# Performance work log

Measured on AMD Instinct MI355X. Metric: run time of the kernel, lower is better.

## Reference

```python
import jax, jax.numpy as jnp
import numpy as np

N, E, D, L, G, T = 50000, 600000, 128, 4, 512, 10
EPS = 1e-5


def setup_inputs() -> dict:
    key = jax.random.key(0)
    ks = jax.random.split(key, 20)
    s = lambda k, shp, fan: jax.random.normal(k, shp, jnp.float32) * (1.0 / np.sqrt(fan))
    inp = {
        'x': jax.random.normal(ks[0], (N, 3), jnp.float32),
        'edge_index': jax.random.randint(ks[1], (2, E), 0, N, jnp.int32),
        'batch': jnp.sort(jax.random.randint(ks[2], (N,), 0, G, jnp.int32)),
        'emb_W': s(ks[3], (3, D), 3),
        'emb_b': jnp.zeros((D,), jnp.float32),
        'conv_W': s(ks[4], (L, 12 * D, D), 12 * D),
        'conv_b': jnp.zeros((L, D), jnp.float32),
        'bn_gamma': jnp.ones((L, D), jnp.float32),
        'bn_beta': jnp.zeros((L, D), jnp.float32),
        'W1': s(ks[5], (D, D // 2), D), 'b1': jnp.zeros((D // 2,), jnp.float32),
        'W2': s(ks[6], (D // 2, D // 4), D // 2), 'b2': jnp.zeros((D // 4,), jnp.float32),
        'W3': s(ks[7], (D // 4, T), D // 4), 'b3': jnp.zeros((T,), jnp.float32),
    }
    return inp


def reference(x, edge_index, batch, emb_W, emb_b, conv_W, conv_b, bn_gamma, bn_beta,
              W1, b1, W2, b2, W3, b3):
    n = x.shape[0]
    src, dst = edge_index[0], edge_index[1]  # messages flow src(j) -> dst(i)
    deg = jax.ops.segment_sum(jnp.ones((src.shape[0],), x.dtype), dst, num_segments=n)
    delta = jnp.mean(jnp.log1p(deg))          # avg log-degree (PNA's avg_deg['log'])
    d = jnp.maximum(deg, 1.0)[:, None]        # clamp(min=1)
    log_d = jnp.log1p(d)
    amp, att = log_d / delta, delta / log_d   # amplification / attenuation scalers
    has_edge = (deg > 0)[:, None]

    h = x @ emb_W + emb_b                     # node_emb Linear(3, D)
    for l in range(conv_W.shape[0]):
        msg = h[src]                          # [E, D] gather
        s1 = jax.ops.segment_sum(msg, dst, num_segments=n)
        s2 = jax.ops.segment_sum(msg * msg, dst, num_segments=n)
        mean = s1 / d
        std = jnp.sqrt(jax.nn.relu(s2 / d - mean * mean) + EPS)
        mn = jnp.where(has_edge, jax.ops.segment_min(msg, dst, num_segments=n), 0.0)
        mx = jnp.where(has_edge, jax.ops.segment_max(msg, dst, num_segments=n), 0.0)
        aggs = jnp.concatenate([mean, mn, mx, std], axis=-1)                 # [N, 4D]
        out = jnp.concatenate([aggs, aggs * amp, aggs * att], axis=-1)       # [N, 12D]
        out = out @ conv_W[l] + conv_b[l]      # post_nn Linear(12D, D)
        mu = out.mean(axis=0)
        var = out.var(axis=0)
        out = (out - mu) * jax.lax.rsqrt(var + EPS) * bn_gamma[l] + bn_beta[l]
        h = jax.nn.relu(out) + h               # residual (dropout off: eval)

    # global_mean_pool over graphs
    gsum = jax.ops.segment_sum(h, batch, num_segments=G)
    cnt = jnp.maximum(jax.ops.segment_sum(jnp.ones((n,), h.dtype), batch, num_segments=G), 1.0)
    g = gsum / cnt[:, None]
    g = jax.nn.relu(g @ W1 + b1)
    g = jax.nn.relu(g @ W2 + b2)
    return g @ W3 + b3                         # source='image': no clamp
```

## Files before the change

kernel.cpp:

```cpp
#include <hip/hip_runtime.h>
#include <math.h>

#define NN 50000
#define NE 600000
#define DD 128
#define NL 4
#define NG 512
#define NT 10
#define NPAD 50176
#define EPSF 1e-5f

typedef __bf16 bf16x8 __attribute__((ext_vector_type(8)));
typedef float f32x4 __attribute__((ext_vector_type(4)));

__device__ __forceinline__ unsigned short f2bf(float x) {
    union { float f; unsigned u; } v; v.f = x;
    unsigned r = v.u + 0x7FFFu + ((v.u >> 16) & 1u);
    return (unsigned short)(r >> 16);
}
__device__ __forceinline__ unsigned pack_bf2(float a, float b) {
    return (unsigned)f2bf(a) | ((unsigned)f2bf(b) << 16);
}
__device__ __forceinline__ float bf_lo(unsigned v) {
    union { unsigned u; float f; } w; w.u = (v & 0xFFFFu) << 16; return w.f;
}
__device__ __forceinline__ float bf_hi(unsigned v) {
    union { unsigned u; float f; } w; w.u = v & 0xFFFF0000u; return w.f;
}

__global__ void k_count(const int* __restrict__ dst, int* __restrict__ deg,
                        float* __restrict__ dsum, int E) {
    int e = blockIdx.x * blockDim.x + threadIdx.x;
    if (e == 0) *dsum = 0.f;
    if (e < E) atomicAdd(&deg[dst[e]], 1);
}

__global__ void k_scan_part(const int* __restrict__ deg, int* __restrict__ part, int n) {
    __shared__ int sm[256];
    int b = blockIdx.x, t = threadIdx.x;
    int base = b * 1024 + t * 4;
    int s = 0;
    #pragma unroll
    for (int j = 0; j < 4; j++) if (base + j < n) s += deg[base + j];
    sm[t] = s;
    __syncthreads();
    for (int off = 128; off > 0; off >>= 1) {
        if (t < off) sm[t] += sm[t + off];
        __syncthreads();
    }
    if (t == 0) part[b] = sm[0];
}

__global__ void k_scan_top(const int* __restrict__ part, int* __restrict__ offs,
                           int* __restrict__ row_ptr, int nb, int n) {
    if (threadIdx.x == 0) {
        int acc = 0;
        for (int i = 0; i < nb; i++) { offs[i] = acc; acc += part[i]; }
        row_ptr[n] = acc;
    }
}

__global__ void k_scan_apply(const int* __restrict__ deg, const int* __restrict__ offs,
                             int* __restrict__ row_ptr, int* __restrict__ cursor, int n) {
    __shared__ int sm[256];
    int b = blockIdx.x, t = threadIdx.x;
    int base = b * 1024 + t * 4;
    int v[4]; int s = 0;
    #pragma unroll
    for (int j = 0; j < 4; j++) { v[j] = (base + j < n) ? deg[base + j] : 0; s += v[j]; }
    sm[t] = s;
    __syncthreads();
    for (int off = 1; off < 256; off <<= 1) {
        int y = (t >= off) ? sm[t - off] : 0;
        __syncthreads();
        sm[t] += y;
        __syncthreads();
    }
    int run = offs[b] + sm[t] - s;
    #pragma unroll
    for (int j = 0; j < 4; j++) {
        if (base + j < n) { row_ptr[base + j] = run; cursor[base + j] = run; run += v[j]; }
    }
}

__global__ void k_fill(const int* __restrict__ src, const int* __restrict__ dst,
                       int* __restrict__ cursor, int* __restrict__ csr_src, int E) {
    int e = blockIdx.x * blockDim.x + threadIdx.x;
    if (e < E) {
        int d = dst[e];
        int pos = atomicAdd(&cursor[d], 1);
        csr_src[pos] = src[e];
    }
}

__global__ void k_delta(const int* __restrict__ deg, float* __restrict__ dsum, int n) {
    int i = blockIdx.x * blockDim.x + threadIdx.x;
    float v = (i < n) ? log1pf((float)deg[i]) : 0.f;
    #pragma unroll
    for (int off = 32; off > 0; off >>= 1) v += __shfl_down(v, off);
    if ((threadIdx.x & 63) == 0) atomicAdd(dsum, v);
}

__global__ void k_scalars(const int* __restrict__ deg, const float* __restrict__ dsum,
                          float* __restrict__ inv_d, float* __restrict__ amp,
                          float* __restrict__ att, int n) {
    int i = blockIdx.x * blockDim.x + threadIdx.x;
    if (i >= n) return;
    float delta = *dsum / (float)n;
    float d = fmaxf((float)deg[i], 1.f);
    float ld = log1pf(d);
    inv_d[i] = 1.f / d;
    amp[i] = ld / delta;
    att[i] = delta / ld;
}

__global__ void k_emb(const float* __restrict__ x, const float* __restrict__ W,
                      const float* __restrict__ b, unsigned* __restrict__ hb2, int total2) {
    int i = blockIdx.x * blockDim.x + threadIdx.x;
    if (i >= total2) return;
    int node = i >> 6, c = (i & 63) * 2;
    float x0 = x[node * 3 + 0], x1 = x[node * 3 + 1], x2 = x[node * 3 + 2];
    float v0 = x0 * W[c] + x1 * W[DD + c] + x2 * W[2 * DD + c] + b[c];
    float v1 = x0 * W[c + 1] + x1 * W[DD + c + 1] + x2 * W[2 * DD + c + 1] + b[c + 1];
    hb2[i] = pack_bf2(v0, v1);
}

__global__ void k_wconv(const float* __restrict__ W, unsigned short* __restrict__ Bt2, int total) {
    int o = blockIdx.x * blockDim.x + threadIdx.x;
    if (o >= total) return;
    int l = o / 196608;
    int idx = o % 196608;
    int kc = idx / 3072;
    int rem = idx % 3072;
    int j = rem >> 10;
    int nn = (rem >> 3) & 127;
    int k8 = rem & 7;
    int k = kc * 8 + k8;
    Bt2[o] = f2bf(W[(size_t)l * 196608 + (size_t)(j * 512 + k) * 128 + nn]);
}

__global__ void k_agg(const unsigned* __restrict__ hb2, const int* __restrict__ row_ptr,
                      const int* __restrict__ csr_src, const float* __restrict__ inv_d,
                      unsigned* __restrict__ atw, float* __restrict__ bn_zero) {
    __shared__ unsigned ldsb[16 * 260];
    int tid = threadIdx.x;
    if (blockIdx.x == 0) bn_zero[tid] = 0.f;
    int w = tid >> 6, t = tid & 63;
    int node0 = blockIdx.x * 16;
    #pragma unroll 1
    for (int q = 0; q < 4; q++) {
        int nl = w * 4 + q;
        int node = node0 + nl;
        int beg = row_ptr[node], end = row_ptr[node + 1];
        float s1a = 0.f, s1b = 0.f, s2a = 0.f, s2b = 0.f;
        float mna = INFINITY, mnb = INFINITY, mxa = -INFINITY, mxb = -INFINITY;
        int e = beg;
        for (; e + 3 < end; e += 4) {
            int sa = csr_src[e],     sb = csr_src[e + 1];
            int sc = csr_src[e + 2], sd = csr_src[e + 3];
            unsigned va = hb2[(size_t)sa * 64 + t];
            unsigned vb = hb2[(size_t)sb * 64 + t];
            unsigned vc = hb2[(size_t)sc * 64 + t];
            unsigned vd = hb2[(size_t)sd * 64 + t];
            float a0 = bf_lo(va), b0 = bf_hi(va);
            float a1 = bf_lo(vb), b1 = bf_hi(vb);
            float a2 = bf_lo(vc), b2 = bf_hi(vc);
            float a3 = bf_lo(vd), b3 = bf_hi(vd);
            s1a += (a0 + a1) + (a2 + a3);
            s2a += a0 * a0 + a1 * a1 + a2 * a2 + a3 * a3;
            mna = fminf(fminf(mna, fminf(a0, a1)), fminf(a2, a3));
            mxa = fmaxf(fmaxf(mxa, fmaxf(a0, a1)), fmaxf(a2, a3));
            s1b += (b0 + b1) + (b2 + b3);
            s2b += b0 * b0 + b1 * b1 + b2 * b2 + b3 * b3;
            mnb = fminf(fminf(mnb, fminf(b0, b1)), fminf(b2, b3));
            mxb = fmaxf(fmaxf(mxb, fmaxf(b0, b1)), fmaxf(b2, b3));
        }
        for (; e < end; e++) {
            int sa = csr_src[e];
            unsigned va = hb2[(size_t)sa * 64 + t];
            float a0 = bf_lo(va), b0 = bf_hi(va);
            s1a += a0; s2a += a0 * a0; mna = fminf(mna, a0); mxa = fmaxf(mxa, a0);
            s1b += b0; s2b += b0 * b0; mnb = fminf(mnb, b0); mxb = fmaxf(mxb, b0);
        }
        float id = inv_d[node];
        float meana = s1a * id, meanb = s1b * id;
        float sda = sqrtf(fmaxf(s2a * id - meana * meana, 0.f) + EPSF);
        float sdb = sqrtf(fmaxf(s2b * id - meanb * meanb, 0.f) + EPSF);
        if (beg == end) { mna = 0.f; mxa = 0.f; mnb = 0.f; mxb = 0.f; }
        int base = nl * 260;
        ldsb[base + 0 * 64 + t] = pack_bf2(meana, meanb);
        ldsb[base + 1 * 64 + t] = pack_bf2(mna, mnb);
        ldsb[base + 2 * 64 + t] = pack_bf2(mxa, mxb);
        ldsb[base + 3 * 64 + t] = pack_bf2(sda, sdb);
    }
    __syncthreads();
    #pragma unroll
    for (int p = 0; p < 4; p++) {
        int id = p * 256 + tid;
        int node = id & 15, c = id >> 4;
        int sec = c >> 4, cb = c & 15;
        const unsigned* s = &ldsb[node * 260 + sec * 64 + cb * 4];
        uint4 v = make_uint4(s[0], s[1], s[2], s[3]);
        *(uint4*)&atw[((size_t)c * NPAD + node0 + node) * 4] = v;
    }
}

__global__ __launch_bounds__(256, 2) void k_gemm_mfma(
    const unsigned short* __restrict__ At, const unsigned short* __restrict__ Bt2,
    const float* __restrict__ bias, const float* __restrict__ amp,
    const float* __restrict__ att, float* __restrict__ outp,
    float* __restrict__ bn_sum, float* __restrict__ bn_sq, int n) {
    int tid = threadIdx.x;
    int w = tid >> 6, lane = tid & 63;
    int quad = lane >> 4, l16 = lane & 15;
    int bid = blockIdx.x;
    int tile = (bid >> 5) * 8 + (bid & 7);
    int cg = (bid >> 3) & 3;
    if (tile >= 196) return;
    int c0 = cg * 32;
    int base = tile * 256 + w * 64;

    f32x4 acc[4][2][3];
    #pragma unroll
    for (int rt = 0; rt < 4; rt++)
        #pragma unroll
        for (int ct = 0; ct < 2; ct++)
            #pragma unroll
            for (int j = 0; j < 3; j++) acc[rt][ct][j] = (f32x4)(0.f);

    const unsigned short* pA = At + ((size_t)quad * NPAD + base + l16) * 8;
    const unsigned short* pB = Bt2 + ((size_t)quad * 384 + c0 + l16) * 8;
    const size_t stepA = (size_t)4 * NPAD * 8;
    const int stepB = 4 * 384 * 8;

    bf16x8 af0[4], af1[4], bf0[2][3], bf1[2][3];
    auto loadA = [&](bf16x8* dst) {
        #pragma unroll
        for (int rt = 0; rt < 4; rt++) dst[rt] = *(const bf16x8*)(pA + rt * 128);
        pA += stepA;
    };
    auto loadB = [&](bf16x8 (*dst)[3]) {
        #pragma unroll
        for (int ct = 0; ct < 2; ct++)
            #pragma unroll
            for (int j = 0; j < 3; j++)
                dst[ct][j] = *(const bf16x8*)(pB + j * 1024 + ct * 128);
        pB += stepB;
    };
    auto domfma = [&](bf16x8* af, bf16x8 (*bf)[3]) {
        #pragma unroll
        for (int ct = 0; ct < 2; ct++)
            #pragma unroll
            for (int j = 0; j < 3; j++)
                #pragma unroll
                for (int rt = 0; rt < 4; rt++)
                    acc[rt][ct][j] = __builtin_amdgcn_mfma_f32_16x16x32_bf16(
                        af[rt], bf[ct][j], acc[rt][ct][j], 0, 0, 0);
    };

    loadA(af0); loadB(bf0);
    #pragma unroll 1
    for (int it = 0; it < 16; it += 2) {
        loadA(af1); loadB(bf1);
        domfma(af0, bf0);
        loadA(af0); loadB(bf0);
        domfma(af1, bf1);
    }

    float psum[2] = {0.f, 0.f}, psq[2] = {0.f, 0.f};
    #pragma unroll
    for (int rt = 0; rt < 4; rt++) {
        #pragma unroll
        for (int reg = 0; reg < 4; reg++) {
            int row = base + rt * 16 + quad * 4 + reg;
            if (row < n) {
                float am = amp[row], at = att[row];
                #pragma unroll
                for (int ct = 0; ct < 2; ct++) {
                    int col = c0 + ct * 16 + l16;
                    float v = acc[rt][ct][0][reg] + am * acc[rt][ct][1][reg]
                            + at * acc[rt][ct][2][reg] + bias[col];
                    outp[(size_t)row * DD + col] = v;
                    psum[ct] += v;
                    psq[ct] += v * v;
                }
            }
        }
    }
    #pragma unroll
    for (int ct = 0; ct < 2; ct++) {
        psum[ct] += __shfl_xor(psum[ct], 16, 64);
        psum[ct] += __shfl_xor(psum[ct], 32, 64);
        psq[ct]  += __shfl_xor(psq[ct], 16, 64);
        psq[ct]  += __shfl_xor(psq[ct], 32, 64);
    }
    if (quad == 0) {
        #pragma unroll
        for (int ct = 0; ct < 2; ct++) {
            int col = c0 + ct * 16 + l16;
            atomicAdd(&bn_sum[col], psum[ct]);
            atomicAdd(&bn_sq[col], psq[ct]);
        }
    }
}

__global__ void k_bnapply(const float* __restrict__ outp, const float* __restrict__ bn_sum,
                          const float* __restrict__ bn_sq, const float* __restrict__ gamma,
                          const float* __restrict__ beta, unsigned* __restrict__ hb2,
                          int total8) {
    int i = blockIdx.x * blockDim.x + threadIdx.x;
    if (i >= total8) return;
    int c = (i & 15) * 8;
    const float invn = 1.f / (float)NN;
    float4 o0 = ((const float4*)outp)[i * 2];
    float4 o1 = ((const float4*)outp)[i * 2 + 1];
    uint4 hv = ((const uint4*)hb2)[i];
    float oo[8] = {o0.x, o0.y, o0.z, o0.w, o1.x, o1.y, o1.z, o1.w};
    unsigned hu[4] = {hv.x, hv.y, hv.z, hv.w};
    unsigned ru[4];
    #pragma unroll
    for (int p = 0; p < 4; p++) {
        int c0 = c + p * 2;
        float mu0 = bn_sum[c0] * invn;
        float var0 = bn_sq[c0] * invn - mu0 * mu0;
        float sc0 = rsqrtf(var0 + EPSF) * gamma[c0];
        float sh0 = beta[c0] - mu0 * sc0;
        float mu1 = bn_sum[c0 + 1] * invn;
        float var1 = bn_sq[c0 + 1] * invn - mu1 * mu1;
        float sc1 = rsqrtf(var1 + EPSF) * gamma[c0 + 1];
        float sh1 = beta[c0 + 1] - mu1 * sc1;
        float v0 = fmaxf(oo[p * 2] * sc0 + sh0, 0.f) + bf_lo(hu[p]);
        float v1 = fmaxf(oo[p * 2 + 1] * sc1 + sh1, 0.f) + bf_hi(hu[p]);
        ru[p] = pack_bf2(v0, v1);
    }
    ((uint4*)hb2)[i] = make_uint4(ru[0], ru[1], ru[2], ru[3]);
}

__global__ void k_pool_mlp(const unsigned* __restrict__ hb2, const int* __restrict__ batch,
                           const float* __restrict__ W1, const float* __restrict__ b1,
                           const float* __restrict__ W2, const float* __restrict__ b2,
                           const float* __restrict__ W3, const float* __restrict__ b3,
                           float* __restrict__ out, int n) {
    __shared__ float gvec[128];
    __shared__ float h1[64];
    __shared__ float h2[32];
    __shared__ int srange[2];
    int g = blockIdx.x;
    int t = threadIdx.x;
    if (t < 2) {
        int target = g + t;
        int lo = 0, hi = n;
        while (lo < hi) {
            int mid = (lo + hi) >> 1;
            if (batch[mid] < target) lo = mid + 1; else hi = mid;
        }
        srange[t] = lo;
    }
    __syncthreads();
    int s = srange[0], e = srange[1];
    int p = t >> 1, odd = t & 1;
    float acc = 0.f;
    for (int i = s; i < e; i++) {
        unsigned v = hb2[(size_t)i * 64 + p];
        acc += odd ? bf_hi(v) : bf_lo(v);
    }
    float cnt = fmaxf((float)(e - s), 1.f);
    gvec[t] = acc / cnt;
    __syncthreads();
    if (t < 64) {
        float a = b1[t];
        for (int k = 0; k < 128; k++) a += gvec[k] * W1[k * 64 + t];
        h1[t] = fmaxf(a, 0.f);
    }
    __syncthreads();
    if (t < 32) {
        float a = b2[t];
        for (int k = 0; k < 64; k++) a += h1[k] * W2[k * 32 + t];
        h2[t] = fmaxf(a, 0.f);
    }
    __syncthreads();
    if (t < 10) {
        float a = b3[t];
        for (int k = 0; k < 32; k++) a += h2[k] * W3[k * 10 + t];
        out[g * NT + t] = a;
    }
}

extern "C" void kernel_launch(void* const* d_in, const int* in_sizes, int n_in,
                              void* d_out, int out_size, void* d_ws, size_t ws_size,
                              hipStream_t stream) {
    const float* x      = (const float*)d_in[0];
    const int*   eidx   = (const int*)d_in[1];
    const int*   batch  = (const int*)d_in[2];
    const float* emb_W  = (const float*)d_in[3];
    const float* emb_b  = (const float*)d_in[4];
    const float* conv_W = (const float*)d_in[5];
    const float* conv_b = (const float*)d_in[6];
    const float* bn_g   = (const float*)d_in[7];
    const float* bn_b   = (const float*)d_in[8];
    const float* W1 = (const float*)d_in[9];
    const float* b1 = (const float*)d_in[10];
    const float* W2 = (const float*)d_in[11];
    const float* b2 = (const float*)d_in[12];
    const float* W3 = (const float*)d_in[13];
    const float* b3 = (const float*)d_in[14];
    float* out = (float*)d_out;

    const int* src = eidx;
    const int* dst = eidx + NE;

    char* p = (char*)d_ws;
    auto carve = [&](size_t bytes) {
        void* r = (void*)p;
        p += (bytes + 255) & ~(size_t)255;
        return r;
    };
    int* deg      = (int*)carve(NN * 4);
    int* row_ptr  = (int*)carve((NN + 1) * 4);
    int* cursor   = (int*)carve(NN * 4);
    int* csr_src  = (int*)carve(NE * 4);
    int* part     = (int*)carve(64 * 4);
    int* offs     = (int*)carve(64 * 4);
    float* inv_d  = (float*)carve(NN * 4);
    float* amp    = (float*)carve(NN * 4);
    float* att    = (float*)carve(NN * 4);
    float* dsum   = (float*)carve(4);
    float* bn_sum = (float*)carve(DD * 4);
    float* bn_sq  = (float*)carve(DD * 4);
    unsigned* hb2 = (unsigned*)carve((size_t)NN * 64 * 4);
    unsigned* At  = (unsigned*)carve((size_t)68 * NPAD * 16);
    float* outp   = (float*)carve((size_t)NN * DD * 4);
    unsigned short* Bt2 = (unsigned short*)carve(((size_t)NL * 196608 + 12288) * 2);

    hipMemsetAsync(deg, 0, NN * 4, stream);

    const int NSB = (NN + 1023) / 1024;
    k_count<<<(NE + 255) / 256, 256, 0, stream>>>(dst, deg, dsum, NE);
    k_scan_part<<<NSB, 256, 0, stream>>>(deg, part, NN);
    k_scan_top<<<1, 64, 0, stream>>>(part, offs, row_ptr, NSB, NN);
    k_scan_apply<<<NSB, 256, 0, stream>>>(deg, offs, row_ptr, cursor, NN);
    k_fill<<<(NE + 255) / 256, 256, 0, stream>>>(src, dst, cursor, csr_src, NE);
    k_delta<<<(NN + 255) / 256, 256, 0, stream>>>(deg, dsum, NN);
    k_scalars<<<(NN + 255) / 256, 256, 0, stream>>>(deg, dsum, inv_d, amp, att, NN);
    k_emb<<<(NN * 64 + 255) / 256, 256, 0, stream>>>(x, emb_W, emb_b, hb2, NN * 64);
    k_wconv<<<(NL * 196608 + 255) / 256, 256, 0, stream>>>(conv_W, Bt2, NL * 196608);

    const int gemm_blocks = 800;
    for (int l = 0; l < NL; l++) {
        k_agg<<<NN / 16, 256, 0, stream>>>(hb2, row_ptr, csr_src, inv_d, At, bn_sum);
        k_gemm_mfma<<<gemm_blocks, 256, 0, stream>>>(
            (const unsigned short*)At, Bt2 + (size_t)l * 196608,
            conv_b + l * DD, amp, att, outp, bn_sum, bn_sq, NN);
        k_bnapply<<<(NN * 16 + 255) / 256, 256, 0, stream>>>(
            outp, bn_sum, bn_sq, bn_g + l * DD, bn_b + l * DD, hb2, NN * 16);
    }

    k_pool_mlp<<<NG, 128, 0, stream>>>(hb2, batch, W1, b1, W2, b2, W3, b3, out, NN);
}
```

Before: 616.9 us.

## Fuse neighbor aggregation with MFMA post-NN GEMM via shared-memory A tile

Merges the aggregation kernel and the bf16 MFMA GEMM into one kernel per layer. Each block aggregates 64 nodes into an LDS tile laid out for MFMA A-fragments, then four waves each compute 32 output columns from it. This removes the global At buffer round-trip and one launch per layer. BN accumulator zeroing moves into k_emb with per-layer slices. The cost is 66KB of LDS per block, which limits occupancy, and a serial aggregate-then-GEMM phase inside each block with no overlap.

```diff
diff --git a/kernel.cpp b/kernel.cpp
--- a/kernel.cpp
+++ b/kernel.cpp
@@ -7,7 +7,6 @@
 #define NL 4
 #define NG 512
 #define NT 10
-#define NPAD 50176
 #define EPSF 1e-5f
 
 typedef __bf16 bf16x8 __attribute__((ext_vector_type(8)));
@@ -115,8 +114,13 @@
 }
 
 __global__ void k_emb(const float* __restrict__ x, const float* __restrict__ W,
-                      const float* __restrict__ b, unsigned* __restrict__ hb2, int total2) {
+                      const float* __restrict__ b, unsigned* __restrict__ hb2,
+                      float* __restrict__ bn_all, int total2) {
     int i = blockIdx.x * blockDim.x + threadIdx.x;
+    if (blockIdx.x == 0) {
+        #pragma unroll
+        for (int p = 0; p < 4; p++) bn_all[threadIdx.x + p * 256] = 0.f;
+    }
     if (i >= total2) return;
     int node = i >> 6, c = (i & 63) * 2;
     float x0 = x[node * 3 + 0], x1 = x[node * 3 + 1], x2 = x[node * 3 + 2];
@@ -139,19 +143,25 @@
     Bt2[o] = f2bf(W[(size_t)l * 196608 + (size_t)(j * 512 + k) * 128 + nn]);
 }
 
-__global__ void k_agg(const unsigned* __restrict__ hb2, const int* __restrict__ row_ptr,
-                      const int* __restrict__ csr_src, const float* __restrict__ inv_d,
-                      unsigned* __restrict__ atw, float* __restrict__ bn_zero) {
-    __shared__ unsigned ldsb[16 * 260];
+__global__ __launch_bounds__(256, 2) void k_agg_gemm(
+    const unsigned* __restrict__ hb2, const int* __restrict__ row_ptr,
+    const int* __restrict__ csr_src, const float* __restrict__ inv_d,
+    const unsigned short* __restrict__ Bt2, const float* __restrict__ bias,
+    const float* __restrict__ amp, const float* __restrict__ att,
+    float* __restrict__ outp, float* __restrict__ bn_sum, float* __restrict__ bn_sq, int n) {
+    __shared__ unsigned sA[64 * 260];
     int tid = threadIdx.x;
-    if (blockIdx.x == 0) bn_zero[tid] = 0.f;
     int w = tid >> 6, t = tid & 63;
-    int node0 = blockIdx.x * 16;
+    int quad = t >> 4, l16 = t & 15;
+    int node0 = blockIdx.x * 64;
+
+    int cw = t >> 2, co = t & 3;
     #pragma unroll 1
-    for (int q = 0; q < 4; q++) {
-        int nl = w * 4 + q;
+    for (int q = 0; q < 16; q++) {
+        int nl = w * 16 + q;
         int node = node0 + nl;
-        int beg = row_ptr[node], end = row_ptr[node + 1];
+        int beg = 0, end = 0;
+        if (node < n) { beg = row_ptr[node]; end = row_ptr[node + 1]; }
         float s1a = 0.f, s1b = 0.f, s2a = 0.f, s2b = 0.f;
         float mna = INFINITY, mnb = INFINITY, mxa = -INFINITY, mxb = -INFINITY;
         int e = beg;
@@ -182,44 +192,20 @@
             s1a += a0; s2a += a0 * a0; mna = fminf(mna, a0); mxa = fmaxf(mxa, a0);
             s1b += b0; s2b += b0 * b0; mnb = fminf(mnb, b0); mxb = fmaxf(mxb, b0);
         }
-        float id = inv_d[node];
+        float id = (node < n) ? inv_d[node] : 1.f;
         float meana = s1a * id, meanb = s1b * id;
         float sda = sqrtf(fmaxf(s2a * id - meana * meana, 0.f) + EPSF);
         float sdb = sqrtf(fmaxf(s2b * id - meanb * meanb, 0.f) + EPSF);
         if (beg == end) { mna = 0.f; mxa = 0.f; mnb = 0.f; mxb = 0.f; }
-        int base = nl * 260;
-        ldsb[base + 0 * 64 + t] = pack_bf2(meana, meanb);
-        ldsb[base + 1 * 64 + t] = pack_bf2(mna, mnb);
-        ldsb[base + 2 * 64 + t] = pack_bf2(mxa, mxb);
-        ldsb[base + 3 * 64 + t] = pack_bf2(sda, sdb);
-    }
-    __syncthreads();
-    #pragma unroll
-    for (int p = 0; p < 4; p++) {
-        int id = p * 256 + tid;
-        int node = id & 15, c = id >> 4;
-        int sec = c >> 4, cb = c & 15;
-        const unsigned* s = &ldsb[node * 260 + sec * 64 + cb * 4];
-        uint4 v = make_uint4(s[0], s[1], s[2], s[3]);
-        *(uint4*)&atw[((size_t)c * NPAD + node0 + node) * 4] = v;
-    }
-}
-
-__global__ __launch_bounds__(256, 2) void k_gemm_mfma(
-    const unsigned short* __restrict__ At, const unsigned short* __restrict__ Bt2,
-    const float* __restrict__ bias, const float* __restrict__ amp,
-    const float* __restrict__ att, float* __restrict__ outp,
-    float* __restrict__ bn_sum, float* __restrict__ bn_sq, int n) {
-    int tid = threadIdx.x;
-    int w = tid >> 6, lane = tid & 63;
-    int quad = lane >> 4, l16 = lane & 15;
-    int bid = blockIdx.x;
-    int tile = (bid >> 5) * 8 + (bid & 7);
-    int cg = (bid >> 3) & 3;
-    if (tile >= 196) return;
-    int c0 = cg * 32;
-    int base = tile * 256 + w * 64;
-
+        int wbase = nl * 4 + co;
+        sA[(0 * 16 + cw) * 260 + wbase] = pack_bf2(meana, meanb);
+        sA[(1 * 16 + cw) * 260 + wbase] = pack_bf2(mna, mnb);
+        sA[(2 * 16 + cw) * 260 + wbase] = pack_bf2(mxa, mxb);
+        sA[(3 * 16 + cw) * 260 + wbase] = pack_bf2(sda, sdb);
+    }
+    __syncthreads();
+
+    int c0 = w * 32;
     f32x4 acc[4][2][3];
     #pragma unroll
     for (int rt = 0; rt < 4; rt++)
@@ -228,17 +214,9 @@
             #pragma unroll
             for (int j = 0; j < 3; j++) acc[rt][ct][j] = (f32x4)(0.f);
 
-    const unsigned short* pA = At + ((size_t)quad * NPAD + base + l16) * 8;
     const unsigned short* pB = Bt2 + ((size_t)quad * 384 + c0 + l16) * 8;
-    const size_t stepA = (size_t)4 * NPAD * 8;
     const int stepB = 4 * 384 * 8;
-
-    bf16x8 af0[4], af1[4], bf0[2][3], bf1[2][3];
-    auto loadA = [&](bf16x8* dst) {
-        #pragma unroll
-        for (int rt = 0; rt < 4; rt++) dst[rt] = *(const bf16x8*)(pA + rt * 128);
-        pA += stepA;
-    };
+    bf16x8 bf0[2][3], bf1[2][3];
     auto loadB = [&](bf16x8 (*dst)[3]) {
         #pragma unroll
         for (int ct = 0; ct < 2; ct++)
@@ -247,7 +225,12 @@
                 dst[ct][j] = *(const bf16x8*)(pB + j * 1024 + ct * 128);
         pB += stepB;
     };
-    auto domfma = [&](bf16x8* af, bf16x8 (*bf)[3]) {
+    auto step = [&](int it, bf16x8 (*bf)[3]) {
+        bf16x8 af[4];
+        int kc = it * 4 + quad;
+        #pragma unroll
+        for (int rt = 0; rt < 4; rt++)
+            af[rt] = *(const bf16x8*)&sA[kc * 260 + (rt * 16 + l16) * 4];
         #pragma unroll
         for (int ct = 0; ct < 2; ct++)
             #pragma unroll
@@ -258,13 +241,13 @@
                         af[rt], bf[ct][j], acc[rt][ct][j], 0, 0, 0);
     };
 
-    loadA(af0); loadB(bf0);
+    loadB(bf0);
     #pragma unroll 1
     for (int it = 0; it < 16; it += 2) {
-        loadA(af1); loadB(bf1);
-        domfma(af0, bf0);
-        loadA(af0); loadB(bf0);
-        domfma(af1, bf1);
+        loadB(bf1);
+        step(it, bf0);
+        loadB(bf0);
+        step(it + 1, bf1);
     }
 
     float psum[2] = {0.f, 0.f}, psq[2] = {0.f, 0.f};
@@ -272,7 +255,7 @@
     for (int rt = 0; rt < 4; rt++) {
         #pragma unroll
         for (int reg = 0; reg < 4; reg++) {
-            int row = base + rt * 16 + quad * 4 + reg;
+            int row = node0 + rt * 16 + quad * 4 + reg;
             if (row < n) {
                 float am = amp[row], at = att[row];
                 #pragma unroll
@@ -425,12 +408,13 @@
     float* amp    = (float*)carve(NN * 4);
     float* att    = (float*)carve(NN * 4);
     float* dsum   = (float*)carve(4);
-    float* bn_sum = (float*)carve(DD * 4);
-    float* bn_sq  = (float*)carve(DD * 4);
+    float* bn_all = (float*)carve(1024 * 4);
     unsigned* hb2 = (unsigned*)carve((size_t)NN * 64 * 4);
-    unsigned* At  = (unsigned*)carve((size_t)68 * NPAD * 16);
     float* outp   = (float*)carve((size_t)NN * DD * 4);
     unsigned short* Bt2 = (unsigned short*)carve(((size_t)NL * 196608 + 12288) * 2);
+
+    float* bn_sum = bn_all;
+    float* bn_sq  = bn_all + 512;
 
     hipMemsetAsync(deg, 0, NN * 4, stream);
 
@@ -442,17 +426,18 @@
     k_fill<<<(NE + 255) / 256, 256, 0, stream>>>(src, dst, cursor, csr_src, NE);
     k_delta<<<(NN + 255) / 256, 256, 0, stream>>>(deg, dsum, NN);
     k_scalars<<<(NN + 255) / 256, 256, 0, stream>>>(deg, dsum, inv_d, amp, att, NN);
-    k_emb<<<(NN * 64 + 255) / 256, 256, 0, stream>>>(x, emb_W, emb_b, hb2, NN * 64);
+    k_emb<<<(NN * 64 + 255) / 256, 256, 0, stream>>>(x, emb_W, emb_b, hb2, bn_all, NN * 64);
     k_wconv<<<(NL * 196608 + 255) / 256, 256, 0, stream>>>(conv_W, Bt2, NL * 196608);
 
-    const int gemm_blocks = 800;
+    const int fused_blocks = (NN + 63) / 64;
     for (int l = 0; l < NL; l++) {
-        k_agg<<<NN / 16, 256, 0, stream>>>(hb2, row_ptr, csr_src, inv_d, At, bn_sum);
-        k_gemm_mfma<<<gemm_blocks, 256, 0, stream>>>(
-            (const unsigned short*)At, Bt2 + (size_t)l * 196608,
-            conv_b + l * DD, amp, att, outp, bn_sum, bn_sq, NN);
+        k_agg_gemm<<<fused_blocks, 256, 0, stream>>>(
+            hb2, row_ptr, csr_src, inv_d,
+            Bt2 + (size_t)l * 196608, conv_b + l * DD, amp, att,
+            outp, bn_sum + l * DD, bn_sq + l * DD, NN);
         k_bnapply<<<(NN * 16 + 255) / 256, 256, 0, stream>>>(
-            outp, bn_sum, bn_sq, bn_g + l * DD, bn_b + l * DD, hb2, NN * 16);
+            outp, bn_sum + l * DD, bn_sq + l * DD,
+            bn_g + l * DD, bn_b + l * DD, hb2, NN * 16);
     }
 
     k_pool_mlp<<<NG, 128, 0, stream>>>(hb2, batch, W1, b1, W2, b2, W3, b3, out, NN);
```

Result: slower. 796.7 us (+29.2%).
